# Kernel tuning notes

Hardware: AMD Instinct MI355X
Metric: run time of the kernel (lower is better)

The kernel has to match this reference:

```python
import jax, jax.numpy as jnp
import numpy as np

D_MODEL = 1024
N_HEADS = 16
D_K = D_MODEL // N_HEADS
B = 2048
S = 20  # hardcoded by the 20x20 decay matrix in the original module


def setup_inputs() -> dict:
    key = jax.random.key(0)
    ks = jax.random.split(key, 8)
    bound = np.sqrt(6.0 / (D_MODEL + D_MODEL))  # xavier_uniform gain=1
    lin_b = 1.0 / np.sqrt(D_MODEL)              # default torch Linear bias init
    Q = jax.random.normal(ks[0], (B, S, D_MODEL), dtype=jnp.float32)
    W_Q = jax.random.uniform(ks[1], (D_MODEL, D_MODEL), jnp.float32, -bound, bound)
    W_K = jax.random.uniform(ks[2], (D_MODEL, D_MODEL), jnp.float32, -bound, bound)
    W_V = jax.random.uniform(ks[3], (D_MODEL, D_MODEL), jnp.float32, -bound, bound)
    b_Q = jax.random.uniform(ks[4], (D_MODEL,), jnp.float32, -lin_b, lin_b)
    b_K = jax.random.uniform(ks[5], (D_MODEL,), jnp.float32, -lin_b, lin_b)
    b_V = jax.random.uniform(ks[6], (D_MODEL,), jnp.float32, -lin_b, lin_b)
    length = jax.random.randint(ks[7], (B,), 1, S + 1, dtype=jnp.int64)
    return {"Q": Q, "W_Q": W_Q, "b_Q": b_Q, "W_K": W_K, "b_K": b_K,
            "W_V": W_V, "b_V": b_V, "length": length}


def reference(Q, W_Q, b_Q, W_K, b_K, W_V, b_V, length):
    # torch Linear: y = x @ W.T + b
    def proj(x, W, b):
        y = x @ W.T + b                              # [B,S,D]
        return y.reshape(B, S, N_HEADS, D_K).transpose(0, 2, 1, 3)  # [B,H,S,dk]

    q = proj(Q, W_Q, b_Q)
    k = proj(Q, W_K, b_K)
    v = proj(Q, W_V, b_V)

    scores = jnp.einsum('bhqd,bhkd->bhqk', q, k) / np.sqrt(D_K)
    scores = jnp.exp(scores)                         # exp normalization, NO max-subtract (faithful)
    # key-side mask: arange(S) < length, broadcast over heads and query dim
    mask = (jnp.arange(S)[None, :] < length[:, None]).astype(scores.dtype)  # [B,S]
    scores = scores * mask[:, None, None, :]
    attn = scores / (jnp.sum(scores, axis=-1, keepdims=True) + 1e-8)
    context = jnp.einsum('bhqk,bhkd->bhqd', attn, v)

    # decay matrix Md[i,j] = -(|i-j|)
    idx = jnp.arange(S)
    Md = -jnp.abs(idx[:, None] - idx[None, :]).astype(context.dtype)  # [S,S]
    deAtt = context + jnp.einsum('qk,bhkd->bhqd', Md, v)

    out = deAtt.transpose(0, 2, 1, 3).reshape(B, S, D_MODEL)
    return out
```

## Files before the change

kernel.cpp:

```cpp
#include <hip/hip_runtime.h>

typedef unsigned short u16;
typedef __attribute__((ext_vector_type(8))) __bf16 bf16x8;
typedef __attribute__((ext_vector_type(4))) float f32x4;
typedef __attribute__((ext_vector_type(16))) float f32x16;

__device__ __forceinline__ u16 f2bf(float x) {
    union { float f; unsigned int u; } v; v.f = x;
    unsigned int r = v.u + 0x7fffu + ((v.u >> 16) & 1u);
    return (u16)(r >> 16);
}

typedef const __attribute__((address_space(1))) void* gas_ptr;
typedef __attribute__((address_space(3))) void* las_ptr;
#define GLOAD_LDS16(g, l) __builtin_amdgcn_global_load_lds((gas_ptr)(const void*)(g), (las_ptr)(void*)(l), 16, 0, 0)

__global__ void cvt_bf16(const float* __restrict__ src, u16* __restrict__ dst, int n8) {
    int i = blockIdx.x * blockDim.x + threadIdx.x;
    if (i >= n8) return;
    const float4* s = (const float4*)src + (size_t)i * 2;
    float4 a = s[0], b = s[1];
    union { u16 u[8]; uint4 v; } o;
    o.u[0] = f2bf(a.x); o.u[1] = f2bf(a.y); o.u[2] = f2bf(a.z); o.u[3] = f2bf(a.w);
    o.u[4] = f2bf(b.x); o.u[5] = f2bf(b.y); o.u[6] = f2bf(b.z); o.u[7] = f2bf(b.w);
    *((uint4*)dst + i) = o.v;
}

__global__ __launch_bounds__(512, 2) void gemm_qkv(
    const u16* __restrict__ X, const u16* __restrict__ W,
    const float* __restrict__ bQ, const float* __restrict__ bK,
    const float* __restrict__ bV, u16* __restrict__ Y)
{
    __shared__ __align__(16) u16 AB[2][2][16384];
    const int tid = threadIdx.x;
    const int w = tid >> 6, lane = tid & 63;
    const int wave_m = w >> 2, wave_n = w & 3;
    const int l15 = lane & 15, l4 = lane >> 4, l7 = lane & 7;

    const int nwg = gridDim.x;
    const int bid = blockIdx.x;
    const int q = nwg >> 3, r = nwg & 7;
    const int xcd = bid & 7, idx = bid >> 3;
    const int swz = (xcd < r ? xcd * (q + 1) : r * (q + 1) + (xcd - r) * q) + idx;
    const int bx = swz % 12, by = swz / 12;
    const size_t mBase = (size_t)by << 8;
    const int nBase = bx << 8;

    const int lr = lane >> 3, lc = lane & 7, lcs = lc ^ lr;
    const u16* gA = X + (mBase + (size_t)(w * 32 + lr)) * 1024 + lcs * 8;
    const u16* gB = W + ((size_t)(nBase + w * 32 + lr)) * 1024 + lcs * 8;
    const int stOff = (w * 32) * 64;

    f32x4 acc[8][4];
#pragma unroll
    for (int mi = 0; mi < 8; ++mi)
#pragma unroll
        for (int ni = 0; ni < 4; ++ni)
#pragma unroll
            for (int rr = 0; rr < 4; ++rr) acc[mi][ni][rr] = 0.f;

#pragma unroll
    for (int j = 0; j < 4; ++j) {
        GLOAD_LDS16(gA + j * 8192, &AB[0][0][stOff + j * 512]);
        GLOAD_LDS16(gB + j * 8192, &AB[0][1][stOff + j * 512]);
    }
    asm volatile("s_waitcnt vmcnt(0)" ::: "memory");
    __builtin_amdgcn_s_barrier();
    __builtin_amdgcn_sched_barrier(0);

    const int aR = wave_m * 128 + l15;
    const int bR = wave_n * 64 + l15;
    const int ck0 = (l4 ^ l7) * 8;
    const int ck1 = ((4 | l4) ^ l7) * 8;

    for (int t = 0; t < 16; ++t) {
        u16* curA = (t & 1) ? &AB[1][0][0] : &AB[0][0][0];
        u16* curB = (t & 1) ? &AB[1][1][0] : &AB[0][1][0];
        u16* stA  = (t & 1) ? &AB[0][0][stOff] : &AB[1][0][stOff];
        u16* stB  = (t & 1) ? &AB[0][1][stOff] : &AB[1][1][stOff];
        const int kNxt = (t + 1) * 64;
        const bool pf = (t < 15);

        bf16x8 a[4], b[4];
#pragma unroll
        for (int ni = 0; ni < 4; ++ni)
            b[ni] = *(const bf16x8*)&curB[(bR + ni * 16) * 64 + ck0];
#pragma unroll
        for (int mi = 0; mi < 4; ++mi)
            a[mi] = *(const bf16x8*)&curA[(aR + mi * 16) * 64 + ck0];
        if (pf) {
            GLOAD_LDS16(gA + kNxt,        stA);
            GLOAD_LDS16(gA + kNxt + 8192, stA + 512);
            GLOAD_LDS16(gB + kNxt,        stB);
            GLOAD_LDS16(gB + kNxt + 8192, stB + 512);
        }
        __builtin_amdgcn_s_barrier();
        __builtin_amdgcn_s_setprio(1);
#pragma unroll
        for (int mi = 0; mi < 4; ++mi)
#pragma unroll
            for (int ni = 0; ni < 4; ++ni)
                acc[mi][ni] = __builtin_amdgcn_mfma_f32_16x16x32_bf16(a[mi], b[ni], acc[mi][ni], 0, 0, 0);
        __builtin_amdgcn_s_setprio(0);
        __builtin_amdgcn_s_barrier();

#pragma unroll
        for (int mi = 0; mi < 4; ++mi)
            a[mi] = *(const bf16x8*)&curA[(aR + (mi + 4) * 16) * 64 + ck0];
        if (pf) {
            GLOAD_LDS16(gA + kNxt + 16384, stA + 1024);
            GLOAD_LDS16(gA + kNxt + 24576, stA + 1536);
            GLOAD_LDS16(gB + kNxt + 16384, stB + 1024);
            GLOAD_LDS16(gB + kNxt + 24576, stB + 1536);
        }
        __builtin_amdgcn_s_barrier();
        __builtin_amdgcn_s_setprio(1);
#pragma unroll
        for (int mi = 0; mi < 4; ++mi)
#pragma unroll
            for (int ni = 0; ni < 4; ++ni)
                acc[mi + 4][ni] = __builtin_amdgcn_mfma_f32_16x16x32_bf16(a[mi], b[ni], acc[mi + 4][ni], 0, 0, 0);
        __builtin_amdgcn_s_setprio(0);
        __builtin_amdgcn_s_barrier();

#pragma unroll
        for (int ni = 0; ni < 4; ++ni)
            b[ni] = *(const bf16x8*)&curB[(bR + ni * 16) * 64 + ck1];
#pragma unroll
        for (int mi = 0; mi < 4; ++mi)
            a[mi] = *(const bf16x8*)&curA[(aR + mi * 16) * 64 + ck1];
        __builtin_amdgcn_s_barrier();
        __builtin_amdgcn_s_setprio(1);
#pragma unroll
        for (int mi = 0; mi < 4; ++mi)
#pragma unroll
            for (int ni = 0; ni < 4; ++ni)
                acc[mi][ni] = __builtin_amdgcn_mfma_f32_16x16x32_bf16(a[mi], b[ni], acc[mi][ni], 0, 0, 0);
        __builtin_amdgcn_s_setprio(0);
        __builtin_amdgcn_s_barrier();

#pragma unroll
        for (int mi = 0; mi < 4; ++mi)
            a[mi] = *(const bf16x8*)&curA[(aR + (mi + 4) * 16) * 64 + ck1];
        __builtin_amdgcn_s_barrier();
        __builtin_amdgcn_s_setprio(1);
#pragma unroll
        for (int mi = 0; mi < 4; ++mi)
#pragma unroll
            for (int ni = 0; ni < 4; ++ni)
                acc[mi + 4][ni] = __builtin_amdgcn_mfma_f32_16x16x32_bf16(a[mi], b[ni], acc[mi + 4][ni], 0, 0, 0);
        __builtin_amdgcn_s_setprio(0);
        asm volatile("s_waitcnt vmcnt(0)" ::: "memory");
        __builtin_amdgcn_s_barrier();
        __builtin_amdgcn_sched_barrier(0);
    }

    const int third = nBase >> 10;
    const float* bias = (third == 0) ? bQ : ((third == 1) ? bK : bV);
    const int bcol = (nBase & 1023) + wave_n * 64 + l15;
    float bv[4];
#pragma unroll
    for (int ni = 0; ni < 4; ++ni) bv[ni] = bias[bcol + ni * 16];
#pragma unroll
    for (int mi = 0; mi < 8; ++mi) {
        size_t rb = mBase + wave_m * 128 + mi * 16 + l4 * 4;
#pragma unroll
        for (int ni = 0; ni < 4; ++ni) {
            int col = nBase + wave_n * 64 + ni * 16 + l15;
#pragma unroll
            for (int rr = 0; rr < 4; ++rr)
                Y[(rb + rr) * 3072 + col] = f2bf(acc[mi][ni][rr] + bv[ni]);
        }
    }
}

__global__ __launch_bounds__(256) void attn_dec(
    const u16* __restrict__ Y, const int* __restrict__ lenp, float* __restrict__ out)
{
    __shared__ __align__(16) u16 coefLds[4][1024];
    __shared__ __align__(16) u16 vLds[4][1280];
    const int tid = threadIdx.x;
    const int w = tid >> 6, lane = tid & 63;
    const int u = blockIdx.x * 4 + w;
    const int b = u >> 4, h = u & 15;
    const int L = lenp[b];
    const int j32 = lane & 31, hw = lane >> 5;
    const int m19 = (j32 < 19) ? j32 : 19;

    const u16* qb = Y + (size_t)b * 61440 + h * 64;
    const u16* kb = qb + 1024;
    const u16* vb = qb + 2048;

    f32x16 s;
    for (int r = 0; r < 16; ++r) s[r] = 0.f;
#pragma unroll
    for (int kc = 0; kc < 4; ++kc) {
        const int off = kc * 16 + hw * 8;
        bf16x8 aq = *(const bf16x8*)(qb + (size_t)m19 * 3072 + off);
        bf16x8 bk = *(const bf16x8*)(kb + (size_t)m19 * 3072 + off);
        s = __builtin_amdgcn_mfma_f32_32x32x16_bf16(aq, bk, s, 0, 0, 0);
    }

#pragma unroll
    for (int t = 0; t < 3; ++t) {
        int c = t * 64 + lane;
        if (c < 160) {
            uint4 d = *(const uint4*)(vb + (size_t)(c >> 3) * 3072 + (c & 7) * 8);
            *(uint4*)&vLds[w][c * 8] = d;
        }
    }

#pragma unroll
    for (int r = 0; r < 16; ++r) {
        int i = (r & 3) + ((r >> 2) << 3) + (hw << 2);
        float ev = (i < 20 && j32 < L) ? __expf(s[r] * 0.125f) : 0.f;
        float sum = ev;
#pragma unroll
        for (int o = 1; o < 32; o <<= 1) sum += __shfl_xor(sum, o, 32);
        float coef = ev / (sum + 1e-8f);
        if (i < 20 && j32 < 20) coef -= (float)((i > j32) ? (i - j32) : (j32 - i));
        if (i >= 20 || j32 >= 20) coef = 0.f;
        coefLds[w][i * 32 + j32] = f2bf(coef);
    }
    __syncthreads();

    f32x16 o0, o1;
    for (int r = 0; r < 16; ++r) { o0[r] = 0.f; o1[r] = 0.f; }
#pragma unroll
    for (int kc = 0; kc < 2; ++kc) {
        bf16x8 ac = *(const bf16x8*)&coefLds[w][j32 * 32 + kc * 16 + hw * 8];
        bf16x8 bv0, bv1;
#pragma unroll
        for (int jj = 0; jj < 8; ++jj) {
            int j = kc * 16 + hw * 8 + jj;
            int jc = (j < 19) ? j : 19;
            bv0[jj] = *(const __bf16*)&vLds[w][jc * 64 + j32];
            bv1[jj] = *(const __bf16*)&vLds[w][jc * 64 + 32 + j32];
        }
        o0 = __builtin_amdgcn_mfma_f32_32x32x16_bf16(ac, bv0, o0, 0, 0, 0);
        o1 = __builtin_amdgcn_mfma_f32_32x32x16_bf16(ac, bv1, o1, 0, 0, 0);
    }

#pragma unroll
    for (int r = 0; r < 16; ++r) {
        int i = (r & 3) + ((r >> 2) << 3) + (hw << 2);
        if (i < 20) {
            size_t ro = ((size_t)b * 20 + i) * 1024 + h * 64 + j32;
            out[ro] = o0[r];
            out[ro + 32] = o1[r];
        }
    }
}

extern "C" void kernel_launch(void* const* d_in, const int* in_sizes, int n_in,
                              void* d_out, int out_size, void* d_ws, size_t ws_size,
                              hipStream_t stream) {
    const float* Q   = (const float*)d_in[0];
    const float* W_Q = (const float*)d_in[1];
    const float* b_Q = (const float*)d_in[2];
    const float* W_K = (const float*)d_in[3];
    const float* b_K = (const float*)d_in[4];
    const float* W_V = (const float*)d_in[5];
    const float* b_V = (const float*)d_in[6];
    const int*   len = (const int*)d_in[7];
    float* out = (float*)d_out;

    int NB = 2048;
    while (NB > 64 && 6291456ull + (unsigned long long)NB * 163840ull > (unsigned long long)ws_size)
        NB >>= 1;
    if (6291456ull + (unsigned long long)NB * 163840ull > (unsigned long long)ws_size)
        return;

    u16* Wbf = (u16*)d_ws;
    u16* Xbf = Wbf + 3145728;
    u16* Yq  = Xbf + (size_t)NB * 20480;

    cvt_bf16<<<512, 256, 0, stream>>>(W_Q, Wbf,           131072);
    cvt_bf16<<<512, 256, 0, stream>>>(W_K, Wbf + 1048576, 131072);
    cvt_bf16<<<512, 256, 0, stream>>>(W_V, Wbf + 2097152, 131072);

    const int nsl = 2048 / NB;
    for (int sI = 0; sI < nsl; ++sI) {
        int bBase = sI * NB;
        cvt_bf16<<<NB * 10, 256, 0, stream>>>(Q + (size_t)bBase * 20480, Xbf, NB * 2560);
        int nwg = 12 * ((NB * 20) >> 8);
        gemm_qkv<<<nwg, 512, 0, stream>>>(Xbf, Wbf, b_Q, b_K, b_V, Yq);
        attn_dec<<<NB * 4, 256, 0, stream>>>(Yq, len + bBase, out + (size_t)bBase * 20480);
    }
}
```

Before: 634.7 us.

## Compute transposed scores to keep attention coefficients in registers, drop LDS round-trip

The score MFMA now uses K as the A operand and Q as B, so each lane holds one query row's scores. The softmax sum then needs a single cross-half shuffle instead of a 5-step butterfly per element. Coefficients are packed to bf16 pairs and exchanged between wave halves with shuffles to build the second MFMA's A operand directly, removing the coefficient LDS buffer and its __syncthreads. V global loads are also issued before the score MFMAs to hide their latency, at the cost of extra registers.

```diff
diff --git a/kernel.cpp b/kernel.cpp
--- a/kernel.cpp
+++ b/kernel.cpp
@@ -9,6 +9,9 @@
     union { float f; unsigned int u; } v; v.f = x;
     unsigned int r = v.u + 0x7fffu + ((v.u >> 16) & 1u);
     return (u16)(r >> 16);
+}
+__device__ __forceinline__ unsigned int pack2bf(float a, float b) {
+    return (unsigned int)f2bf(a) | ((unsigned int)f2bf(b) << 16);
 }
 
 typedef const __attribute__((address_space(1))) void* gas_ptr;
@@ -177,65 +180,98 @@
 __global__ __launch_bounds__(256) void attn_dec(
     const u16* __restrict__ Y, const int* __restrict__ lenp, float* __restrict__ out)
 {
-    __shared__ __align__(16) u16 coefLds[4][1024];
     __shared__ __align__(16) u16 vLds[4][1280];
     const int tid = threadIdx.x;
     const int w = tid >> 6, lane = tid & 63;
     const int u = blockIdx.x * 4 + w;
     const int b = u >> 4, h = u & 15;
     const int L = lenp[b];
-    const int j32 = lane & 31, hw = lane >> 5;
-    const int m19 = (j32 < 19) ? j32 : 19;
+    const int i32 = lane & 31, hw = lane >> 5;
+    const int m19 = (i32 < 19) ? i32 : 19;
 
     const u16* qb = Y + (size_t)b * 61440 + h * 64;
     const u16* kb = qb + 1024;
     const u16* vb = qb + 2048;
 
+    uint4 vReg[3];
+    int vC[3];
+#pragma unroll
+    for (int t = 0; t < 3; ++t) {
+        int c = t * 64 + lane;
+        vC[t] = c;
+        if (c < 160)
+            vReg[t] = *(const uint4*)(vb + (size_t)(c >> 3) * 3072 + (c & 7) * 8);
+    }
+
     f32x16 s;
     for (int r = 0; r < 16; ++r) s[r] = 0.f;
 #pragma unroll
     for (int kc = 0; kc < 4; ++kc) {
         const int off = kc * 16 + hw * 8;
-        bf16x8 aq = *(const bf16x8*)(qb + (size_t)m19 * 3072 + off);
-        bf16x8 bk = *(const bf16x8*)(kb + (size_t)m19 * 3072 + off);
-        s = __builtin_amdgcn_mfma_f32_32x32x16_bf16(aq, bk, s, 0, 0, 0);
-    }
-
-#pragma unroll
-    for (int t = 0; t < 3; ++t) {
-        int c = t * 64 + lane;
-        if (c < 160) {
-            uint4 d = *(const uint4*)(vb + (size_t)(c >> 3) * 3072 + (c & 7) * 8);
-            *(uint4*)&vLds[w][c * 8] = d;
-        }
-    }
-
+        bf16x8 ak = *(const bf16x8*)(kb + (size_t)m19 * 3072 + off);
+        bf16x8 bq = *(const bf16x8*)(qb + (size_t)m19 * 3072 + off);
+        s = __builtin_amdgcn_mfma_f32_32x32x16_bf16(ak, bq, s, 0, 0, 0);
+    }
+
+#pragma unroll
+    for (int t = 0; t < 3; ++t)
+        if (vC[t] < 160) *(uint4*)&vLds[w][vC[t] * 8] = vReg[t];
+
+    float ev[16];
+    float part = 0.f;
 #pragma unroll
     for (int r = 0; r < 16; ++r) {
-        int i = (r & 3) + ((r >> 2) << 3) + (hw << 2);
-        float ev = (i < 20 && j32 < L) ? __expf(s[r] * 0.125f) : 0.f;
-        float sum = ev;
-#pragma unroll
-        for (int o = 1; o < 32; o <<= 1) sum += __shfl_xor(sum, o, 32);
-        float coef = ev / (sum + 1e-8f);
-        if (i < 20 && j32 < 20) coef -= (float)((i > j32) ? (i - j32) : (j32 - i));
-        if (i >= 20 || j32 >= 20) coef = 0.f;
-        coefLds[w][i * 32 + j32] = f2bf(coef);
-    }
-    __syncthreads();
+        int j = (r & 3) + ((r >> 2) << 3) + (hw << 2);
+        float e = (i32 < 20 && j < L) ? __expf(s[r] * 0.125f) : 0.f;
+        ev[r] = e;
+        part += e;
+    }
+    float sum = part + __shfl_xor(part, 32, 64);
+    float inv = 1.f / (sum + 1e-8f);
+
+    unsigned int wOwn[8];
+#pragma unroll
+    for (int p = 0; p < 8; ++p) {
+        float c01[2];
+#pragma unroll
+        for (int q2 = 0; q2 < 2; ++q2) {
+            int r = 2 * p + q2;
+            int j = (r & 3) + ((r >> 2) << 3) + (hw << 2);
+            float c = ev[r] * inv;
+            if (i32 < 20 && j < 20)
+                c -= (float)((i32 > j) ? (i32 - j) : (j - i32));
+            else
+                c = 0.f;
+            c01[q2] = c;
+        }
+        wOwn[p] = pack2bf(c01[0], c01[1]);
+    }
+    unsigned int wPar[8];
+#pragma unroll
+    for (int p = 0; p < 8; ++p)
+        wPar[p] = (unsigned int)__shfl_xor((int)wOwn[p], 32, 64);
+
+    union { unsigned int u[4]; bf16x8 v; } A0, A1;
+    if (hw == 0) {
+        A0.u[0] = wOwn[0]; A0.u[1] = wOwn[1]; A0.u[2] = wPar[0]; A0.u[3] = wPar[1];
+        A1.u[0] = wOwn[4]; A1.u[1] = wOwn[5]; A1.u[2] = wPar[4]; A1.u[3] = wPar[5];
+    } else {
+        A0.u[0] = wPar[2]; A0.u[1] = wPar[3]; A0.u[2] = wOwn[2]; A0.u[3] = wOwn[3];
+        A1.u[0] = wPar[6]; A1.u[1] = wPar[7]; A1.u[2] = wOwn[6]; A1.u[3] = wOwn[7];
+    }
 
     f32x16 o0, o1;
     for (int r = 0; r < 16; ++r) { o0[r] = 0.f; o1[r] = 0.f; }
 #pragma unroll
     for (int kc = 0; kc < 2; ++kc) {
-        bf16x8 ac = *(const bf16x8*)&coefLds[w][j32 * 32 + kc * 16 + hw * 8];
+        bf16x8 ac = (kc == 0) ? A0.v : A1.v;
         bf16x8 bv0, bv1;
 #pragma unroll
         for (int jj = 0; jj < 8; ++jj) {
             int j = kc * 16 + hw * 8 + jj;
             int jc = (j < 19) ? j : 19;
-            bv0[jj] = *(const __bf16*)&vLds[w][jc * 64 + j32];
-            bv1[jj] = *(const __bf16*)&vLds[w][jc * 64 + 32 + j32];
+            bv0[jj] = *(const __bf16*)&vLds[w][jc * 64 + i32];
+            bv1[jj] = *(const __bf16*)&vLds[w][jc * 64 + 32 + i32];
         }
         o0 = __builtin_amdgcn_mfma_f32_32x32x16_bf16(ac, bv0, o0, 0, 0, 0);
         o1 = __builtin_amdgcn_mfma_f32_32x32x16_bf16(ac, bv1, o1, 0, 0, 0);
@@ -245,7 +281,7 @@
     for (int r = 0; r < 16; ++r) {
         int i = (r & 3) + ((r >> 2) << 3) + (hw << 2);
         if (i < 20) {
-            size_t ro = ((size_t)b * 20 + i) * 1024 + h * 64 + j32;
+            size_t ro = ((size_t)b * 20 + i) * 1024 + h * 64 + i32;
             out[ro] = o0[r];
             out[ro + 32] = o1[r];
         }
```

Result: no change. 636.5 us (+0.3%).
